# Optimization experiments

Hardware: AMD Instinct MI355X
Metric: run time of the kernel (lower is better)

The kernel has to match this reference:

```python
import jax, jax.numpy as jnp
import numpy as np

B, C, H, W = 4, 64, 64, 128


def setup_inputs() -> dict:
    key = jax.random.key(0)
    ks = jax.random.split(key, 10)
    s = 1.0 / np.sqrt(C)
    return {
        "query": jax.random.normal(ks[0], (B, C, H, W), dtype=jnp.float32),
        "key_": jax.random.normal(ks[1], (B, C, H, W), dtype=jnp.float32),
        "value": jax.random.normal(ks[2], (B, C, H, W), dtype=jnp.float32),
        "Wq": jax.random.normal(ks[3], (C, C), dtype=jnp.float32) * s,
        "bq": jax.random.normal(ks[4], (C,), dtype=jnp.float32) * s,
        "Wk": jax.random.normal(ks[5], (C, C), dtype=jnp.float32) * s,
        "bk": jax.random.normal(ks[6], (C,), dtype=jnp.float32) * s,
        "Wv": jax.random.normal(ks[7], (C, C), dtype=jnp.float32) * s,
        "bv": jax.random.normal(ks[8], (C,), dtype=jnp.float32) * s,
        "gamma": jax.random.normal(ks[9], (), dtype=jnp.float32) * 0.1,
    }


def reference(query, key_, value, Wq, bq, Wk, bk, Wv, bv, gamma):
    b, c, h, w = query.shape
    n = h * w
    fq = query.reshape(b, c, n)
    fk = key_.reshape(b, c, n)
    fv = value.reshape(b, c, n)
    # 1x1 Conv1d == per-position channel matmul: [C_out, C_in] x [B, C_in, N]
    q = jnp.einsum('oc,bcn->bon', Wq, fq) + bq[:, None]
    k = jnp.einsum('oc,bcn->bon', Wk, fk) + bk[:, None]
    v = jnp.einsum('oc,bcn->bon', Wv, fv) + bv[:, None]
    # query permuted to [B, N, C], bmm with key [B, C, N] -> [B, Nq, Nk]; scale by W (last dim of input shape)
    qk = jnp.einsum('bcn,bcm->bnm', q, k) / w
    # non-standard softmax over dim=1 (query-position axis)
    attn = jax.nn.softmax(qk, axis=1)
    # value [B, C, N] @ attn [B, Nq, Nk] -> [B, C, Nk]
    av = jnp.einsum('bcn,bnm->bcm', v, attn)
    out = gamma * av.reshape(b, c, h, w) + v.reshape(b, c, h, w)
    return out
```

## Files before the change

kernel.cpp:

```cpp
#include <hip/hip_runtime.h>

#define NPOS 8192
#define NC 64
#define NB 4
#define NSPLIT 3
#define NCHUNK 2752
#define QSCALE 0.01127105500167846f

typedef __bf16 bf16x8 __attribute__((ext_vector_type(8)));
typedef __bf16 bf16x4 __attribute__((ext_vector_type(4)));
typedef float f32x4 __attribute__((ext_vector_type(4)));

#define EXP2F(x) __builtin_amdgcn_exp2f(x)

static __device__ __forceinline__ unsigned f2bf_u(float x) {
  unsigned u = __float_as_uint(x);
  return (u + 0x7FFFu + ((u >> 16) & 1u)) >> 16;
}
static __device__ __forceinline__ unsigned pack2(float a, float b) {
  return f2bf_u(a) | (f2bf_u(b) << 16);
}

static __device__ __forceinline__ void gload_lds16(const void* gsrc, void* lds_base) {
  __builtin_amdgcn_global_load_lds(
      (const __attribute__((address_space(1))) unsigned int*)gsrc,
      (__attribute__((address_space(3))) unsigned int*)lds_base, 16, 0, 0);
}

__global__ __launch_bounds__(256) void proj_kernel(
    const float* __restrict__ xq, const float* __restrict__ xk, const float* __restrict__ xv,
    const float* __restrict__ Wq, const float* __restrict__ bq,
    const float* __restrict__ Wk, const float* __restrict__ bk,
    const float* __restrict__ Wv, const float* __restrict__ bv,
    unsigned short* __restrict__ qT, unsigned short* __restrict__ kT,
    unsigned short* __restrict__ vb, float* __restrict__ vf)
{
  __shared__ float sW[NC * NC];
  __shared__ float sB[NC];
  const int p = blockIdx.z, b = blockIdx.y;
  const int n0 = blockIdx.x * 256;
  const int tid = threadIdx.x;
  const int wv = tid >> 6, l = tid & 63;

  const float* x    = p == 0 ? xq : (p == 1 ? xk : xv);
  const float* W    = p == 0 ? Wq : (p == 1 ? Wk : Wv);
  const float* bias = p == 0 ? bq : (p == 1 ? bk : bv);

  for (int i = tid; i < NC * NC; i += 256) sW[i] = W[i];
  if (tid < NC) sB[tid] = bias[tid];
  __syncthreads();

  const int nb = n0 + 4 * l;
  const float* xb = x + (size_t)b * NC * NPOS + nb;

  float acc[16][4];
#pragma unroll
  for (int oi = 0; oi < 16; ++oi) {
    float bz = sB[16 * wv + oi];
    acc[oi][0] = bz; acc[oi][1] = bz; acc[oi][2] = bz; acc[oi][3] = bz;
  }
  for (int c = 0; c < NC; ++c) {
    const float4 x4 = *(const float4*)(xb + (size_t)c * NPOS);
#pragma unroll
    for (int oi = 0; oi < 16; ++oi) {
      float wgt = sW[(16 * wv + oi) * NC + c];
      acc[oi][0] = fmaf(wgt, x4.x, acc[oi][0]);
      acc[oi][1] = fmaf(wgt, x4.y, acc[oi][1]);
      acc[oi][2] = fmaf(wgt, x4.z, acc[oi][2]);
      acc[oi][3] = fmaf(wgt, x4.w, acc[oi][3]);
    }
  }

  if (p < 2) {
    const float qs = (p == 0) ? QSCALE : 1.0f;
    unsigned short* dst = (p == 0 ? qT : kT) + (size_t)b * NPOS * NC;
#pragma unroll
    for (int r = 0; r < 4; ++r) {
      uint4 w0, w1;
      w0.x = pack2(qs * acc[0][r],  qs * acc[1][r]);
      w0.y = pack2(qs * acc[2][r],  qs * acc[3][r]);
      w0.z = pack2(qs * acc[4][r],  qs * acc[5][r]);
      w0.w = pack2(qs * acc[6][r],  qs * acc[7][r]);
      w1.x = pack2(qs * acc[8][r],  qs * acc[9][r]);
      w1.y = pack2(qs * acc[10][r], qs * acc[11][r]);
      w1.z = pack2(qs * acc[12][r], qs * acc[13][r]);
      w1.w = pack2(qs * acc[14][r], qs * acc[15][r]);
      unsigned short* rp = dst + (size_t)(nb + r) * NC + 16 * wv;
      *(uint4*)(rp) = w0;
      *(uint4*)(rp + 8) = w1;
    }
  } else {
#pragma unroll
    for (int oi = 0; oi < 16; ++oi) {
      const int o = 16 * wv + oi;
      float4 v4;
      v4.x = acc[oi][0]; v4.y = acc[oi][1]; v4.z = acc[oi][2]; v4.w = acc[oi][3];
      *(float4*)(vf + ((size_t)b * NC + o) * NPOS + nb) = v4;
      uint2 u2;
      u2.x = pack2(acc[oi][0], acc[oi][1]);
      u2.y = pack2(acc[oi][2], acc[oi][3]);
      *(uint2*)(vb + ((size_t)b * NC + o) * NPOS + nb) = u2;
    }
  }
}

__global__ __launch_bounds__(512) void attn_partial(
    const unsigned short* __restrict__ qT,
    const unsigned short* __restrict__ kT,
    const unsigned short* __restrict__ vb,
    float* __restrict__ pav, float* __restrict__ plsum)
{
  __shared__ unsigned short qs_[2][64 * 64];
  __shared__ unsigned short vs_[2][64 * 64];
  __shared__ unsigned short pT[8][16][72];

  const int b = blockIdx.y, z = blockIdx.z;
  const int m0 = blockIdx.x * 128;
  const int tid = threadIdx.x;
  const int w = tid >> 6, l = tid & 63;
  const int lm = l & 15, g = l >> 4;
  const int m = m0 + 16 * w + lm;

  const unsigned short* kb_p = kT + (size_t)(b * NPOS + m) * NC + 8 * g;
  const bf16x8 kb0 = *(const bf16x8*)(kb_p);
  const bf16x8 kb1 = *(const bf16x8*)(kb_p + 32);

  const char* qb  = (const char*)(qT + (size_t)b * NPOS * NC);
  const char* vbb = (const char*)(vb + (size_t)b * NC * NPOS);

  const int srow = tid >> 3;
  const int slc  = ((tid & 7) * 16) ^ ((srow & 7) << 4);
  const char* qsrc0 = qb + (size_t)srow * 128 + slc;
  const char* vsrc0 = vbb + (size_t)srow * (NPOS * 2) + slc;
  const int ldsoff = w * 512;

  f32x4 acc[4] = {{0,0,0,0},{0,0,0,0},{0,0,0,0},{0,0,0,0}};
  float lsum = 0.f;

  const int nbeg = z * NCHUNK;
  const int nend = (nbeg + NCHUNK < NPOS) ? nbeg + NCHUNK : NPOS;
  const int iters = (nend - nbeg) >> 6;

  gload_lds16(qsrc0 + (size_t)nbeg * 128, &qs_[0][ldsoff]);
  gload_lds16(vsrc0 + (size_t)nbeg * 2,   &vs_[0][ldsoff]);
  __syncthreads();

  const int swz = (lm & 7) << 4;

  int cur = 0;
  for (int t = 0; t < iters; ++t) {
    const int n0 = nbeg + 64 * t;
    if (t + 1 < iters) {
      gload_lds16(qsrc0 + (size_t)(n0 + 64) * 128, &qs_[cur ^ 1][ldsoff]);
      gload_lds16(vsrc0 + (size_t)(n0 + 64) * 2,   &vs_[cur ^ 1][ldsoff]);
    }
    const unsigned short* qt = qs_[cur];
    const unsigned short* vt = vs_[cur];

    f32x4 s[4];
#pragma unroll
    for (int sub = 0; sub < 4; ++sub) {
      const int nl = 16 * sub + lm;
      bf16x8 qa0 = *(const bf16x8*)(qt + nl * 64 + (((16 * g) ^ swz) >> 1));
      bf16x8 qa1 = *(const bf16x8*)(qt + nl * 64 + (((64 + 16 * g) ^ swz) >> 1));
      f32x4 zz = {0, 0, 0, 0};
      zz = __builtin_amdgcn_mfma_f32_16x16x32_bf16(qa0, kb0, zz, 0, 0, 0);
      zz = __builtin_amdgcn_mfma_f32_16x16x32_bf16(qa1, kb1, zz, 0, 0, 0);
      s[sub] = zz;
    }
#pragma unroll
    for (int sub = 0; sub < 4; ++sub) {
      float p0 = EXP2F(s[sub][0]);
      float p1 = EXP2F(s[sub][1]);
      float p2 = EXP2F(s[sub][2]);
      float p3 = EXP2F(s[sub][3]);
      lsum += (p0 + p1) + (p2 + p3);
      bf16x4 pk;
      pk[0] = (__bf16)p0; pk[1] = (__bf16)p1;
      pk[2] = (__bf16)p2; pk[3] = (__bf16)p3;
      *(bf16x4*)&pT[w][lm][16 * sub + 4 * g] = pk;
    }
#pragma unroll
    for (int ks = 0; ks < 2; ++ks) {
      bf16x8 pb = *(const bf16x8*)&pT[w][lm][8 * g + 32 * ks];
#pragma unroll
      for (int cs = 0; cs < 4; ++cs) {
        const int vr = 16 * cs + lm;
        bf16x8 va = *(const bf16x8*)(vt + vr * 64 + (((16 * g + 64 * ks) ^ swz) >> 1));
        acc[cs] = __builtin_amdgcn_mfma_f32_16x16x32_bf16(va, pb, acc[cs], 0, 0, 0);
      }
    }
    __syncthreads();
    cur ^= 1;
  }

  lsum += __shfl_xor(lsum, 16);
  lsum += __shfl_xor(lsum, 32);
  if (l < 16) plsum[((size_t)(z * NB + b) << 13) + m] = lsum;

  float* po = pav + ((size_t)((z * NB + b) * NC) << 13);
#pragma unroll
  for (int cs = 0; cs < 4; ++cs) {
#pragma unroll
    for (int r = 0; r < 4; ++r) {
      const int c = 16 * cs + 4 * g + r;
      po[((size_t)c << 13) + m] = acc[cs][r];
    }
  }
}

__global__ __launch_bounds__(256) void reduce_kernel(
    const float* __restrict__ pav, const float* __restrict__ plsum,
    const float* __restrict__ vf, const float* __restrict__ gamma_p,
    float* __restrict__ out)
{
  const size_t base = ((size_t)blockIdx.x * 256 + threadIdx.x) * 4;
  const int m = (int)(base & (NPOS - 1));
  const int bc = (int)(base >> 13);
  const int b = bc >> 6;

  float4 s = {0, 0, 0, 0};
  float4 L = {0, 0, 0, 0};
#pragma unroll
  for (int zz = 0; zz < NSPLIT; ++zz) {
    const float4 a = *(const float4*)(pav + (((size_t)(zz * NB * NC + bc)) << 13) + m);
    s.x += a.x; s.y += a.y; s.z += a.z; s.w += a.w;
    const float4 q = *(const float4*)(plsum + (((size_t)(zz * NB + b)) << 13) + m);
    L.x += q.x; L.y += q.y; L.z += q.z; L.w += q.w;
  }
  const float gmv = gamma_p[0];
  const float4 v4 = *(const float4*)(vf + base);
  float4 o;
  o.x = gmv * s.x / L.x + v4.x;
  o.y = gmv * s.y / L.y + v4.y;
  o.z = gmv * s.z / L.z + v4.z;
  o.w = gmv * s.w / L.w + v4.w;
  *(float4*)(out + base) = o;
}

extern "C" void kernel_launch(void* const* d_in, const int* in_sizes, int n_in,
                              void* d_out, int out_size, void* d_ws, size_t ws_size,
                              hipStream_t stream) {
  const float* xq = (const float*)d_in[0];
  const float* xk = (const float*)d_in[1];
  const float* xv = (const float*)d_in[2];
  const float* Wq = (const float*)d_in[3];
  const float* bq = (const float*)d_in[4];
  const float* Wk = (const float*)d_in[5];
  const float* bk = (const float*)d_in[6];
  const float* Wv = (const float*)d_in[7];
  const float* bv = (const float*)d_in[8];
  const float* gm = (const float*)d_in[9];
  float* out = (float*)d_out;

  unsigned short* qT   = (unsigned short*)d_ws;
  unsigned short* kT   = qT + (size_t)NB * NPOS * NC;
  unsigned short* vbuf = kT + (size_t)NB * NPOS * NC;
  float* vf    = (float*)(vbuf + (size_t)NB * NPOS * NC);
  float* pav   = vf + (size_t)NB * NC * NPOS;
  float* plsum = pav + (size_t)NSPLIT * NB * NC * NPOS;

  hipLaunchKernelGGL(proj_kernel, dim3(32, 4, 3), dim3(256), 0, stream,
                     xq, xk, xv, Wq, bq, Wk, bk, Wv, bv, qT, kT, vbuf, vf);
  hipLaunchKernelGGL(attn_partial, dim3(NPOS / 128, NB, NSPLIT), dim3(512), 0, stream,
                     qT, kT, vbuf, pav, plsum);
  hipLaunchKernelGGL(reduce_kernel, dim3(2048), dim3(256), 0, stream,
                     pav, plsum, vf, gm, out);
}
```

Measured before the change: 121.0 us.

## Split projection into more blocks and hand-schedule attention loop barriers and priorities

The projection kernel now covers 128 positions per block instead of 256, doubling the grid to give more parallelism and fewer registers per thread. In the attention loop the trailing __syncthreads is replaced by explicit s_barrier pairs, with s_waitcnt vmcnt so the async global-to-LDS prefetch of the next tile is waited on precisely. s_setprio raises wave priority around the MFMA sections. The pT LDS padding changes from 72 to 68. The hand-placed waits and barriers risk subtle LDS races if the vmcnt accounting is off.

```diff
diff --git a/kernel.cpp b/kernel.cpp
--- a/kernel.cpp
+++ b/kernel.cpp
@@ -38,7 +38,7 @@
   __shared__ float sW[NC * NC];
   __shared__ float sB[NC];
   const int p = blockIdx.z, b = blockIdx.y;
-  const int n0 = blockIdx.x * 256;
+  const int n0 = blockIdx.x * 128;
   const int tid = threadIdx.x;
   const int wv = tid >> 6, l = tid & 63;
 
@@ -50,24 +50,22 @@
   if (tid < NC) sB[tid] = bias[tid];
   __syncthreads();
 
-  const int nb = n0 + 4 * l;
+  const int nb = n0 + 2 * l;
   const float* xb = x + (size_t)b * NC * NPOS + nb;
 
-  float acc[16][4];
+  float acc[16][2];
 #pragma unroll
   for (int oi = 0; oi < 16; ++oi) {
     float bz = sB[16 * wv + oi];
-    acc[oi][0] = bz; acc[oi][1] = bz; acc[oi][2] = bz; acc[oi][3] = bz;
+    acc[oi][0] = bz; acc[oi][1] = bz;
   }
   for (int c = 0; c < NC; ++c) {
-    const float4 x4 = *(const float4*)(xb + (size_t)c * NPOS);
+    const float2 x2 = *(const float2*)(xb + (size_t)c * NPOS);
 #pragma unroll
     for (int oi = 0; oi < 16; ++oi) {
       float wgt = sW[(16 * wv + oi) * NC + c];
-      acc[oi][0] = fmaf(wgt, x4.x, acc[oi][0]);
-      acc[oi][1] = fmaf(wgt, x4.y, acc[oi][1]);
-      acc[oi][2] = fmaf(wgt, x4.z, acc[oi][2]);
-      acc[oi][3] = fmaf(wgt, x4.w, acc[oi][3]);
+      acc[oi][0] = fmaf(wgt, x2.x, acc[oi][0]);
+      acc[oi][1] = fmaf(wgt, x2.y, acc[oi][1]);
     }
   }
 
@@ -75,7 +73,7 @@
     const float qs = (p == 0) ? QSCALE : 1.0f;
     unsigned short* dst = (p == 0 ? qT : kT) + (size_t)b * NPOS * NC;
 #pragma unroll
-    for (int r = 0; r < 4; ++r) {
+    for (int r = 0; r < 2; ++r) {
       uint4 w0, w1;
       w0.x = pack2(qs * acc[0][r],  qs * acc[1][r]);
       w0.y = pack2(qs * acc[2][r],  qs * acc[3][r]);
@@ -93,13 +91,10 @@
 #pragma unroll
     for (int oi = 0; oi < 16; ++oi) {
       const int o = 16 * wv + oi;
-      float4 v4;
-      v4.x = acc[oi][0]; v4.y = acc[oi][1]; v4.z = acc[oi][2]; v4.w = acc[oi][3];
-      *(float4*)(vf + ((size_t)b * NC + o) * NPOS + nb) = v4;
-      uint2 u2;
-      u2.x = pack2(acc[oi][0], acc[oi][1]);
-      u2.y = pack2(acc[oi][2], acc[oi][3]);
-      *(uint2*)(vb + ((size_t)b * NC + o) * NPOS + nb) = u2;
+      float2 v2;
+      v2.x = acc[oi][0]; v2.y = acc[oi][1];
+      *(float2*)(vf + ((size_t)b * NC + o) * NPOS + nb) = v2;
+      *(unsigned*)(vb + ((size_t)b * NC + o) * NPOS + nb) = pack2(acc[oi][0], acc[oi][1]);
     }
   }
 }
@@ -112,7 +107,7 @@
 {
   __shared__ unsigned short qs_[2][64 * 64];
   __shared__ unsigned short vs_[2][64 * 64];
-  __shared__ unsigned short pT[8][16][72];
+  __shared__ unsigned short pT[8][16][68];
 
   const int b = blockIdx.y, z = blockIdx.z;
   const int m0 = blockIdx.x * 128;
@@ -143,21 +138,28 @@
 
   gload_lds16(qsrc0 + (size_t)nbeg * 128, &qs_[0][ldsoff]);
   gload_lds16(vsrc0 + (size_t)nbeg * 2,   &vs_[0][ldsoff]);
-  __syncthreads();
 
   const int swz = (lm & 7) << 4;
 
   int cur = 0;
   for (int t = 0; t < iters; ++t) {
     const int n0 = nbeg + 64 * t;
+    __builtin_amdgcn_s_barrier();
     if (t + 1 < iters) {
       gload_lds16(qsrc0 + (size_t)(n0 + 64) * 128, &qs_[cur ^ 1][ldsoff]);
       gload_lds16(vsrc0 + (size_t)(n0 + 64) * 2,   &vs_[cur ^ 1][ldsoff]);
-    }
+      asm volatile("s_waitcnt vmcnt(2)" ::: "memory");
+    } else {
+      asm volatile("s_waitcnt vmcnt(0)" ::: "memory");
+    }
+    __builtin_amdgcn_s_barrier();
+    __builtin_amdgcn_sched_barrier(0);
+
     const unsigned short* qt = qs_[cur];
     const unsigned short* vt = vs_[cur];
 
     f32x4 s[4];
+    __builtin_amdgcn_s_setprio(1);
 #pragma unroll
     for (int sub = 0; sub < 4; ++sub) {
       const int nl = 16 * sub + lm;
@@ -168,6 +170,7 @@
       zz = __builtin_amdgcn_mfma_f32_16x16x32_bf16(qa1, kb1, zz, 0, 0, 0);
       s[sub] = zz;
     }
+    __builtin_amdgcn_s_setprio(0);
 #pragma unroll
     for (int sub = 0; sub < 4; ++sub) {
       float p0 = EXP2F(s[sub][0]);
@@ -180,6 +183,7 @@
       pk[2] = (__bf16)p2; pk[3] = (__bf16)p3;
       *(bf16x4*)&pT[w][lm][16 * sub + 4 * g] = pk;
     }
+    __builtin_amdgcn_s_setprio(1);
 #pragma unroll
     for (int ks = 0; ks < 2; ++ks) {
       bf16x8 pb = *(const bf16x8*)&pT[w][lm][8 * g + 32 * ks];
@@ -190,7 +194,7 @@
         acc[cs] = __builtin_amdgcn_mfma_f32_16x16x32_bf16(va, pb, acc[cs], 0, 0, 0);
       }
     }
-    __syncthreads();
+    __builtin_amdgcn_s_setprio(0);
     cur ^= 1;
   }
 
@@ -260,7 +264,7 @@
   float* pav   = vf + (size_t)NB * NC * NPOS;
   float* plsum = pav + (size_t)NSPLIT * NB * NC * NPOS;
 
-  hipLaunchKernelGGL(proj_kernel, dim3(32, 4, 3), dim3(256), 0, stream,
+  hipLaunchKernelGGL(proj_kernel, dim3(64, 4, 3), dim3(256), 0, stream,
                      xq, xk, xv, Wq, bq, Wk, bk, Wv, bv, qT, kT, vbuf, vf);
   hipLaunchKernelGGL(attn_partial, dim3(NPOS / 128, NB, NSPLIT), dim3(512), 0, stream,
                      qT, kT, vbuf, pav, plsum);
```

Result: faster. 115.2 us (-4.8%).
